# Optimization experiments

Hardware: AMD Instinct MI355X
Metric: run time of the kernel (lower is better)

Reference implementation:

```python
import jax, jax.numpy as jnp
import numpy as np

B, S, D = 4, 2048, 1024
E, H, TOPK = 8, 4096, 2


def setup_inputs() -> dict:
    key = jax.random.key(0)
    ks = jax.random.split(key, 6)
    scale_d = 1.0 / np.sqrt(D)
    scale_h = 1.0 / np.sqrt(H)
    return {
        "x": jax.random.normal(ks[0], (B, S, D), dtype=jnp.float32),
        "gate_w": jax.random.normal(ks[1], (D, E), dtype=jnp.float32) * scale_d,
        "w1": jax.random.normal(ks[2], (E, D, H), dtype=jnp.float32) * scale_d,
        "b1": jnp.zeros((E, H), dtype=jnp.float32),
        "w2": jax.random.normal(ks[3], (E, H, D), dtype=jnp.float32) * scale_h,
        "b2": jnp.zeros((E, D), dtype=jnp.float32),
    }


def reference(x, gate_w, w1, b1, w2, b2):
    # Gate: logits [B, S, E], top-k routing, softmax over the k selected logits
    gate_logits = jnp.einsum("bsd,de->bse", x, gate_w)
    topw, sel = jax.lax.top_k(gate_logits, TOPK)          # [B, S, K]
    topw = jax.nn.softmax(topw.astype(jnp.float32), axis=-1).astype(x.dtype)

    out = jnp.zeros_like(x)
    # Loop over the small, fixed expert set (structurally distinct params).
    for i in range(E):
        # combine weight for expert i per token (0 if not routed to i)
        coef = jnp.sum(jnp.where(sel == i, topw, jnp.zeros((), x.dtype)), axis=-1)  # [B, S]
        h = jax.nn.gelu(jnp.einsum("bsd,dh->bsh", x, w1[i]) + b1[i])
        y = jnp.einsum("bsh,hd->bsd", h, w2[i]) + b2[i]
        out = out + coef[..., None] * y
    return out
```

## Files before the change

kernel.cpp:

```cpp
#include <hip/hip_runtime.h>
#include <hip/hip_bf16.h>

#define T_TOKENS 8192
#define D_DIM 1024
#define H_DIM 4096
#define E_NUM 8
#define CAP 8192
#define CNT_PAD 16

#define TPB_G 32
#define GATE_BLKS (T_TOKENS / TPB_G)
#define TRW1_BLKS ((D_DIM / 64) * (H_DIM / 64) * E_NUM)
#define TRW2_BLKS ((H_DIM / 64) * (D_DIM / 64) * E_NUM)

typedef short bf16x8 __attribute__((ext_vector_type(8)));
typedef float f32x4 __attribute__((ext_vector_type(4)));
typedef unsigned short u16x8 __attribute__((ext_vector_type(8)));

__device__ inline unsigned short f2bf(float f) {
    __hip_bfloat16 h = __float2bfloat16(f);
    return *reinterpret_cast<unsigned short*>(&h);
}

__device__ inline float gelu_sig(float v) {
    float x = v * (1.5957691216057308f + 0.07135481627f * v * v);
    return v * __builtin_amdgcn_rcpf(1.0f + __expf(-x));
}

__device__ inline void gld_lds16(const unsigned short* g, unsigned short* lds) {
    __builtin_amdgcn_global_load_lds(
        (const __attribute__((address_space(1))) void*)g,
        (__attribute__((address_space(3))) void*)lds, 16, 0, 0);
}

#define WAITV0 do { asm volatile("s_waitcnt vmcnt(0)" ::: "memory"); \
                    __builtin_amdgcn_sched_barrier(0); } while (0)
#define SBAR   do { __builtin_amdgcn_sched_barrier(0); \
                    __builtin_amdgcn_s_barrier(); \
                    __builtin_amdgcn_sched_barrier(0); } while (0)

#define XCD_ITEMS(T)                                                          \
    int xcd = blockIdx.x & 7;                                                 \
    int lb  = blockIdx.x >> 3;                                                \
    int nbx = gridDim.x >> 3;                                                 \
    int q_ = (T) >> 3, r_ = (T) & 7;                                          \
    int base_ = (xcd < r_) ? xcd * (q_ + 1) : r_ * (q_ + 1) + (xcd - r_) * q_;\
    int cntx_ = (xcd < r_) ? q_ + 1 : q_;

__device__ inline void trw_body(const float* __restrict__ w,
                                unsigned short* __restrict__ wt,
                                int K, int N, int bb,
                                unsigned short (*tb)[72]) {
    int nk = K / 64, nn = N / 64;
    int e = bb / (nk * nn);
    int rem = bb - e * (nk * nn);
    int k0 = (rem % nk) * 64;
    int n0 = (rem / nk) * 64;
    const float* we = w + (size_t)e * K * N + (size_t)k0 * N + n0;
    unsigned short* wte = wt + (size_t)e * K * N + (size_t)n0 * K + k0;
    int tid = threadIdx.x;

    int kg = tid >> 4;
    int nq = (tid & 15) * 4;
    float4 r0 = *(const float4*)(we + (size_t)(kg * 4 + 0) * N + nq);
    float4 r1 = *(const float4*)(we + (size_t)(kg * 4 + 1) * N + nq);
    float4 r2 = *(const float4*)(we + (size_t)(kg * 4 + 2) * N + nq);
    float4 r3 = *(const float4*)(we + (size_t)(kg * 4 + 3) * N + nq);
    ushort4 u;
    u.x = f2bf(r0.x); u.y = f2bf(r1.x); u.z = f2bf(r2.x); u.w = f2bf(r3.x);
    *(ushort4*)&tb[nq + 0][kg * 4] = u;
    u.x = f2bf(r0.y); u.y = f2bf(r1.y); u.z = f2bf(r2.y); u.w = f2bf(r3.y);
    *(ushort4*)&tb[nq + 1][kg * 4] = u;
    u.x = f2bf(r0.z); u.y = f2bf(r1.z); u.z = f2bf(r2.z); u.w = f2bf(r3.z);
    *(ushort4*)&tb[nq + 2][kg * 4] = u;
    u.x = f2bf(r0.w); u.y = f2bf(r1.w); u.z = f2bf(r2.w); u.w = f2bf(r3.w);
    *(ushort4*)&tb[nq + 3][kg * 4] = u;

    __syncthreads();

#pragma unroll
    for (int p = 0; p < 2; ++p) {
        int n = p * 32 + (tid >> 3);
        int kc = (tid & 7) * 8;
        u16x8 v = *(const u16x8*)&tb[n][kc];
        *(u16x8*)(wte + (size_t)n * K + kc) = v;
    }
}

__global__ __launch_bounds__(256) void prep_kernel(const float* __restrict__ x,
                                                   const float* __restrict__ gw,
                                                   const float* __restrict__ w1,
                                                   const float* __restrict__ w2,
                                                   int* __restrict__ cnt,
                                                   int* __restrict__ tok,
                                                   float* __restrict__ cf,
                                                   unsigned short* __restrict__ xb,
                                                   unsigned short* __restrict__ w1t,
                                                   unsigned short* __restrict__ w2t) {
    __shared__ __align__(16) unsigned short tb[64][72];
    __shared__ int ls0[TPB_G], ls1[TPB_G];
    __shared__ float lp0[TPB_G], lp1[TPB_G];
    int b = blockIdx.x;
    if (b >= GATE_BLKS) {
        int bb = b - GATE_BLKS;
        if (bb < TRW1_BLKS) trw_body(w1, w1t, D_DIM, H_DIM, bb, tb);
        else                trw_body(w2, w2t, H_DIM, D_DIM, bb - TRW1_BLKS, tb);
        return;
    }
    int tid = threadIdx.x;
    int lane = tid & 63, wv = tid >> 6;
#pragma unroll
    for (int rep = 0; rep < TPB_G / 4; ++rep) {
        int ti = rep * 4 + wv;
        int t = b * TPB_G + ti;
        const float* xr = x + (size_t)t * D_DIM;
        unsigned short* xbr = xb + (size_t)t * D_DIM;
        double acc[E_NUM];
#pragma unroll
        for (int e = 0; e < E_NUM; ++e) acc[e] = 0.0;
#pragma unroll
        for (int it = 0; it < 4; ++it) {
            int d = it * 256 + lane * 4;
            float4 v = *(const float4*)(xr + d);
            ushort4 u;
            u.x = f2bf(v.x); u.y = f2bf(v.y); u.z = f2bf(v.z); u.w = f2bf(v.w);
            *(ushort4*)(xbr + d) = u;
            const float vv[4] = {v.x, v.y, v.z, v.w};
#pragma unroll
            for (int j = 0; j < 4; ++j) {
                const float* g = gw + (size_t)(d + j) * E_NUM;
#pragma unroll
                for (int e = 0; e < E_NUM; ++e) acc[e] += (double)vv[j] * (double)g[e];
            }
        }
#pragma unroll
        for (int e = 0; e < E_NUM; ++e) {
            double v = acc[e];
#pragma unroll
            for (int off = 32; off >= 1; off >>= 1) v += __shfl_xor(v, off);
            acc[e] = v;
        }
        if (lane == 0) {
            int s0 = 0;
#pragma unroll
            for (int e = 1; e < E_NUM; ++e) if (acc[e] > acc[s0]) s0 = e;
            int s1 = -1;
#pragma unroll
            for (int e = 0; e < E_NUM; ++e) if (e != s0 && (s1 < 0 || acc[e] > acc[s1])) s1 = e;
            float l0 = (float)acc[s0], l1 = (float)acc[s1];
            float p1 = __expf(l1 - l0);
            float inv = 1.0f / (1.0f + p1);
            ls0[ti] = s0; ls1[ti] = s1;
            lp0[ti] = inv; lp1[ti] = p1 * inv;
        }
    }
    __syncthreads();
    if (tid < E_NUM) {
        int e = tid, c = 0;
#pragma unroll
        for (int i = 0; i < TPB_G; ++i) c += (ls0[i] == e) + (ls1[i] == e);
        if (c > 0) {
            int q = atomicAdd(&cnt[e * CNT_PAD], c);
            for (int i = 0; i < TPB_G; ++i) {
                int t = b * TPB_G + i;
                if (ls0[i] == e) { tok[e * CAP + q] = t; cf[e * CAP + q] = lp0[i]; ++q; }
                if (ls1[i] == e) { tok[e * CAP + q] = t; cf[e * CAP + q] = lp1[i]; ++q; }
            }
        }
    }
}

__global__ __launch_bounds__(256, 2) void gemm1_fast(const unsigned short* __restrict__ xb,
                                                     const unsigned short* __restrict__ w1t,
                                                     const float* __restrict__ b1,
                                                     const int* __restrict__ cnt,
                                                     const int* __restrict__ tok,
                                                     unsigned short* __restrict__ Hbuf) {
    __shared__ __align__(16) unsigned short As0[128][64], As1[128][64];
    __shared__ __align__(16) unsigned short Bs0[128][64], Bs1[128][64];
    __shared__ int s_tok[128];

    int tid = threadIdx.x, lane = tid & 63, wv = tid >> 6;
    int wr = (wv >> 1) * 64, wc = (wv & 1) * 64;
    int lm = lane & 15, lk = lane >> 4;
    int srow = lane >> 3;
    int schunk = ((lane & 7) ^ srow) << 3;

    int ne_[E_NUM], offs_[E_NUM], pref[E_NUM + 1];
    pref[0] = 0;
    int off = 0;
#pragma unroll
    for (int e = 0; e < E_NUM; ++e) {
        ne_[e] = cnt[e * CNT_PAD];
        offs_[e] = off; off += ne_[e];
        pref[e + 1] = pref[e] + ((ne_[e] + 127) >> 7) * 32;
    }
    int T = pref[E_NUM];

    XCD_ITEMS(T)
    for (int ii = lb; ii < cntx_; ii += nbx) {
        int w = base_ + ii;
        int e = 0;
#pragma unroll
        for (int q = 0; q < E_NUM - 1; ++q) e += (w >= pref[q + 1]) ? 1 : 0;
        int local = w - pref[e];
        int bm0 = (local >> 5) * 128;
        int n0 = (local & 31) * 128;
        int ne = ne_[e];
        int offs = offs_[e];
        const unsigned short* w1e = w1t + (size_t)e * H_DIM * D_DIM;

        __syncthreads();
        if (tid < 128) s_tok[tid] = tok[e * CAP + min(bm0 + tid, ne - 1)];
        __syncthreads();

        const unsigned short* gA[4];
        const unsigned short* gB[4];
#pragma unroll
        for (int l = 0; l < 4; ++l) {
            gA[l] = xb + (size_t)s_tok[wv * 32 + l * 8 + srow] * D_DIM + schunk;
            gB[l] = w1e + (size_t)(n0 + wv * 32 + l * 8 + srow) * D_DIM + schunk;
        }
        float bias_v[4];
#pragma unroll
        for (int j = 0; j < 4; ++j) bias_v[j] = b1[(size_t)e * H_DIM + n0 + wc + j * 16 + lm];

        f32x4 acc[4][4];
#pragma unroll
        for (int i = 0; i < 4; ++i)
#pragma unroll
            for (int j = 0; j < 4; ++j) { f32x4 z = {0.f, 0.f, 0.f, 0.f}; acc[i][j] = z; }

        auto STAGE = [&](unsigned short (&A)[128][64], unsigned short (&B)[128][64], int kb) {
            int k0 = kb * 64;
#pragma unroll
            for (int l = 0; l < 4; ++l) gld_lds16(gA[l] + k0, &A[wv * 32 + l * 8][0]);
#pragma unroll
            for (int l = 0; l < 4; ++l) gld_lds16(gB[l] + k0, &B[wv * 32 + l * 8][0]);
        };
        auto COMPUTE = [&](unsigned short (&A)[128][64], unsigned short (&B)[128][64]) {
#pragma unroll
            for (int ks = 0; ks < 2; ++ks) {
                bf16x8 a[4], b[4];
                int c = (((ks * 4 + lk) ^ (lm & 7)) << 3);
#pragma unroll
                for (int f = 0; f < 4; ++f) a[f] = *(const bf16x8*)&A[wr + f * 16 + lm][c];
#pragma unroll
                for (int f = 0; f < 4; ++f) b[f] = *(const bf16x8*)&B[wc + f * 16 + lm][c];
                __builtin_amdgcn_s_setprio(1);
#pragma unroll
                for (int i = 0; i < 4; ++i)
#pragma unroll
                    for (int j = 0; j < 4; ++j)
                        acc[i][j] = __builtin_amdgcn_mfma_f32_16x16x32_bf16(a[i], b[j], acc[i][j], 0, 0, 0);
                __builtin_amdgcn_s_setprio(0);
            }
        };

        const int NT = D_DIM / 64;
        STAGE(As0, Bs0, 0);
        WAITV0; SBAR;
        for (int t = 0; t < NT; t += 2) {
            if (t + 1 < NT) STAGE(As1, Bs1, t + 1);
            COMPUTE(As0, Bs0);
            WAITV0; SBAR;
            if (t + 2 < NT) STAGE(As0, Bs0, t + 2);
            COMPUTE(As1, Bs1);
            WAITV0; SBAR;
        }

#pragma unroll
        for (int i = 0; i < 4; ++i) {
#pragma unroll
            for (int r = 0; r < 4; ++r) {
                int row = wr + i * 16 + lk * 4 + r;
                int gr = bm0 + row;
                if (gr >= ne) continue;
                size_t rb = (size_t)(offs + gr) * H_DIM;
#pragma unroll
                for (int j = 0; j < 4; ++j) {
                    int gn = n0 + wc + j * 16 + lm;
                    float v = acc[i][j][r] + bias_v[j];
                    Hbuf[rb + gn] = f2bf(gelu_sig(v));
                }
            }
        }
    }
}

__global__ __launch_bounds__(256, 2) void gemm2_fast(const unsigned short* __restrict__ Hbuf,
                                                     const unsigned short* __restrict__ w2t,
                                                     const float* __restrict__ b2,
                                                     const int* __restrict__ cnt,
                                                     const int* __restrict__ tok,
                                                     const float* __restrict__ cf,
                                                     float* __restrict__ out) {
    __shared__ __align__(16) unsigned short As0[128][64], As1[128][64];
    __shared__ __align__(16) unsigned short Bs0[128][64], Bs1[128][64];
    __shared__ int s_tok[128];
    __shared__ float s_cf[128];

    int tid = threadIdx.x, lane = tid & 63, wv = tid >> 6;
    int wr = (wv >> 1) * 64, wc = (wv & 1) * 64;
    int lm = lane & 15, lk = lane >> 4;
    int srow = lane >> 3;
    int schunk = ((lane & 7) ^ srow) << 3;

    int ne_[E_NUM], offs_[E_NUM], pref[E_NUM + 1];
    pref[0] = 0;
    int off = 0;
#pragma unroll
    for (int e = 0; e < E_NUM; ++e) {
        ne_[e] = cnt[e * CNT_PAD];
        offs_[e] = off; off += ne_[e];
        pref[e + 1] = pref[e] + ((ne_[e] + 127) >> 7) * 8;
    }
    int T = pref[E_NUM];

    XCD_ITEMS(T)
    for (int ii = lb; ii < cntx_; ii += nbx) {
        int w = base_ + ii;
        int e = 0;
#pragma unroll
        for (int q = 0; q < E_NUM - 1; ++q) e += (w >= pref[q + 1]) ? 1 : 0;
        int local = w - pref[e];
        int bm0 = (local >> 3) * 128;
        int n0 = (local & 7) * 128;
        int ne = ne_[e];
        int offs = offs_[e];
        const unsigned short* w2e = w2t + (size_t)e * H_DIM * D_DIM;

        __syncthreads();
        if (tid < 128) {
            int gi = min(bm0 + tid, ne - 1);
            s_tok[tid] = tok[e * CAP + gi];
            s_cf[tid] = cf[e * CAP + gi];
        }
        __syncthreads();

        const unsigned short* gA[4];
        const unsigned short* gB[4];
#pragma unroll
        for (int l = 0; l < 4; ++l) {
            gA[l] = Hbuf + (size_t)(offs + min(bm0 + wv * 32 + l * 8 + srow, ne - 1)) * H_DIM + schunk;
            gB[l] = w2e + (size_t)(n0 + wv * 32 + l * 8 + srow) * H_DIM + schunk;
        }
        float bias_v[4];
#pragma unroll
        for (int j = 0; j < 4; ++j) bias_v[j] = b2[(size_t)e * D_DIM + n0 + wc + j * 16 + lm];

        f32x4 acc[4][4];
#pragma unroll
        for (int i = 0; i < 4; ++i)
#pragma unroll
            for (int j = 0; j < 4; ++j) { f32x4 z = {0.f, 0.f, 0.f, 0.f}; acc[i][j] = z; }

        auto STAGE = [&](unsigned short (&A)[128][64], unsigned short (&B)[128][64], int kb) {
            int k0 = kb * 64;
#pragma unroll
            for (int l = 0; l < 4; ++l) gld_lds16(gA[l] + k0, &A[wv * 32 + l * 8][0]);
#pragma unroll
            for (int l = 0; l < 4; ++l) gld_lds16(gB[l] + k0, &B[wv * 32 + l * 8][0]);
        };
        auto COMPUTE = [&](unsigned short (&A)[128][64], unsigned short (&B)[128][64]) {
#pragma unroll
            for (int ks = 0; ks < 2; ++ks) {
                bf16x8 a[4], b[4];
                int c = (((ks * 4 + lk) ^ (lm & 7)) << 3);
#pragma unroll
                for (int f = 0; f < 4; ++f) a[f] = *(const bf16x8*)&A[wr + f * 16 + lm][c];
#pragma unroll
                for (int f = 0; f < 4; ++f) b[f] = *(const bf16x8*)&B[wc + f * 16 + lm][c];
                __builtin_amdgcn_s_setprio(1);
#pragma unroll
                for (int i = 0; i < 4; ++i)
#pragma unroll
                    for (int j = 0; j < 4; ++j)
                        acc[i][j] = __builtin_amdgcn_mfma_f32_16x16x32_bf16(a[i], b[j], acc[i][j], 0, 0, 0);
                __builtin_amdgcn_s_setprio(0);
            }
        };

        const int NT = H_DIM / 64;
        STAGE(As0, Bs0, 0);
        WAITV0; SBAR;
        for (int t = 0; t < NT; t += 2) {
            if (t + 1 < NT) STAGE(As1, Bs1, t + 1);
            COMPUTE(As0, Bs0);
            WAITV0; SBAR;
            if (t + 2 < NT) STAGE(As0, Bs0, t + 2);
            COMPUTE(As1, Bs1);
            WAITV0; SBAR;
        }

#pragma unroll
        for (int i = 0; i < 4; ++i) {
#pragma unroll
            for (int r = 0; r < 4; ++r) {
                int row = wr + i * 16 + lk * 4 + r;
                int gr = bm0 + row;
                if (gr >= ne) continue;
                int tk = s_tok[row];
                float cw = s_cf[row];
#pragma unroll
                for (int j = 0; j < 4; ++j) {
                    int gn = n0 + wc + j * 16 + lm;
                    float y = acc[i][j][r] + bias_v[j];
                    atomicAdd(&out[(size_t)tk * D_DIM + gn], cw * y);
                }
            }
        }
    }
}

extern "C" void kernel_launch(void* const* d_in, const int* in_sizes, int n_in,
                              void* d_out, int out_size, void* d_ws, size_t ws_size,
                              hipStream_t stream) {
    const float* x  = (const float*)d_in[0];
    const float* gw = (const float*)d_in[1];
    const float* w1 = (const float*)d_in[2];
    const float* b1 = (const float*)d_in[3];
    const float* w2 = (const float*)d_in[4];
    const float* b2 = (const float*)d_in[5];
    float* out = (float*)d_out;

    char* ws = (char*)d_ws;
    const size_t SZ_CNT   = E_NUM * CNT_PAD * 4;
    const size_t SZ_ROUTE = SZ_CNT + (size_t)2 * E_NUM * CAP * 4;
    const size_t SZ_XB    = (size_t)T_TOKENS * D_DIM * 2;
    const size_t SZ_W     = (size_t)E_NUM * D_DIM * H_DIM * 2;
    const size_t SZ_H     = (size_t)2 * T_TOKENS * H_DIM * 2;

    int*   cnt = (int*)ws;
    int*   tok = (int*)(ws + SZ_CNT);
    float* cff = (float*)(ws + SZ_CNT + E_NUM * CAP * 4);

    size_t need_fast = SZ_ROUTE + SZ_XB + 2 * SZ_W + SZ_H;
    if (ws_size < need_fast) return;

    unsigned short* xb   = (unsigned short*)(ws + SZ_ROUTE);
    unsigned short* w1t  = (unsigned short*)(ws + SZ_ROUTE + SZ_XB);
    unsigned short* w2t  = (unsigned short*)(ws + SZ_ROUTE + SZ_XB + SZ_W);
    unsigned short* Hbuf = (unsigned short*)(ws + SZ_ROUTE + SZ_XB + 2 * SZ_W);

    hipMemsetAsync(cnt, 0, SZ_CNT, stream);
    hipMemsetAsync(out, 0, (size_t)out_size * sizeof(float), stream);

    prep_kernel<<<GATE_BLKS + TRW1_BLKS + TRW2_BLKS, 256, 0, stream>>>(
        x, gw, w1, w2, cnt, tok, cff, xb, w1t, w2t);

    gemm1_fast<<<512, 256, 0, stream>>>(xb, w1t, b1, cnt, tok, Hbuf);
    gemm2_fast<<<512, 256, 0, stream>>>(Hbuf, w2t, b2, cnt, tok, cff, out);
}
```

Baseline: 580.6 us.

## Use 256x256 tiles with 8 waves and triple-buffered K=32 LDS pipeline

```diff
diff --git a/kernel.cpp b/kernel.cpp
--- a/kernel.cpp
+++ b/kernel.cpp
@@ -33,11 +33,13 @@
         (__attribute__((address_space(3))) void*)lds, 16, 0, 0);
 }
 
-#define WAITV0 do { asm volatile("s_waitcnt vmcnt(0)" ::: "memory"); \
-                    __builtin_amdgcn_sched_barrier(0); } while (0)
-#define SBAR   do { __builtin_amdgcn_sched_barrier(0); \
-                    __builtin_amdgcn_s_barrier(); \
-                    __builtin_amdgcn_sched_barrier(0); } while (0)
+#define WAITV(N) do { asm volatile("s_waitcnt vmcnt(" #N ")" ::: "memory"); \
+                      __builtin_amdgcn_sched_barrier(0); } while (0)
+#define LGKM0    do { asm volatile("s_waitcnt lgkmcnt(0)" ::: "memory"); \
+                      __builtin_amdgcn_sched_barrier(0); } while (0)
+#define SBAR     do { __builtin_amdgcn_sched_barrier(0); \
+                      __builtin_amdgcn_s_barrier(); \
+                      __builtin_amdgcn_sched_barrier(0); } while (0)
 
 #define XCD_ITEMS(T)                                                          \
     int xcd = blockIdx.x & 7;                                                 \
@@ -170,21 +172,23 @@
     }
 }
 
-__global__ __launch_bounds__(256, 2) void gemm1_fast(const unsigned short* __restrict__ xb,
+
+__global__ __launch_bounds__(512, 2) void gemm1_fast(const unsigned short* __restrict__ xb,
                                                      const unsigned short* __restrict__ w1t,
                                                      const float* __restrict__ b1,
                                                      const int* __restrict__ cnt,
                                                      const int* __restrict__ tok,
                                                      unsigned short* __restrict__ Hbuf) {
-    __shared__ __align__(16) unsigned short As0[128][64], As1[128][64];
-    __shared__ __align__(16) unsigned short Bs0[128][64], Bs1[128][64];
-    __shared__ int s_tok[128];
+    __shared__ __align__(16) unsigned short As[3][256][32];
+    __shared__ __align__(16) unsigned short Bs[3][256][32];
+    __shared__ int s_tok[256];
 
     int tid = threadIdx.x, lane = tid & 63, wv = tid >> 6;
-    int wr = (wv >> 1) * 64, wc = (wv & 1) * 64;
-    int lm = lane & 15, lk = lane >> 4;
-    int srow = lane >> 3;
-    int schunk = ((lane & 7) ^ srow) << 3;
+    int wm = wv >> 2, wn = wv & 3;
+    int lm = lane & 15, lkq = lane >> 4;
+    int srow = tid >> 2;
+    int schunk = (((tid & 3) ^ (srow & 3)) << 3);
+    int rdc = ((lkq ^ (lm & 3)) << 3);
 
     int ne_[E_NUM], offs_[E_NUM], pref[E_NUM + 1];
     pref[0] = 0;
@@ -193,7 +197,7 @@
     for (int e = 0; e < E_NUM; ++e) {
         ne_[e] = cnt[e * CNT_PAD];
         offs_[e] = off; off += ne_[e];
-        pref[e + 1] = pref[e] + ((ne_[e] + 127) >> 7) * 32;
+        pref[e + 1] = pref[e] + ((ne_[e] + 255) >> 8) * 16;
     }
     int T = pref[E_NUM];
 
@@ -204,82 +208,93 @@
 #pragma unroll
         for (int q = 0; q < E_NUM - 1; ++q) e += (w >= pref[q + 1]) ? 1 : 0;
         int local = w - pref[e];
-        int bm0 = (local >> 5) * 128;
-        int n0 = (local & 31) * 128;
+        int bm0 = (local >> 4) * 256;
+        int n0 = (local & 15) * 256;
         int ne = ne_[e];
         int offs = offs_[e];
         const unsigned short* w1e = w1t + (size_t)e * H_DIM * D_DIM;
 
         __syncthreads();
-        if (tid < 128) s_tok[tid] = tok[e * CAP + min(bm0 + tid, ne - 1)];
+        if (tid < 256) s_tok[tid] = tok[e * CAP + min(bm0 + tid, ne - 1)];
         __syncthreads();
 
-        const unsigned short* gA[4];
-        const unsigned short* gB[4];
-#pragma unroll
-        for (int l = 0; l < 4; ++l) {
-            gA[l] = xb + (size_t)s_tok[wv * 32 + l * 8 + srow] * D_DIM + schunk;
-            gB[l] = w1e + (size_t)(n0 + wv * 32 + l * 8 + srow) * D_DIM + schunk;
+        const unsigned short* gA[2];
+        const unsigned short* gB[2];
+#pragma unroll
+        for (int u = 0; u < 2; ++u) {
+            gA[u] = xb + (size_t)s_tok[u * 128 + srow] * D_DIM + schunk;
+            gB[u] = w1e + (size_t)(n0 + u * 128 + srow) * D_DIM + schunk;
         }
         float bias_v[4];
 #pragma unroll
-        for (int j = 0; j < 4; ++j) bias_v[j] = b1[(size_t)e * H_DIM + n0 + wc + j * 16 + lm];
-
-        f32x4 acc[4][4];
-#pragma unroll
-        for (int i = 0; i < 4; ++i)
+        for (int j = 0; j < 4; ++j)
+            bias_v[j] = b1[(size_t)e * H_DIM + n0 + wn * 64 + j * 16 + lm];
+
+        f32x4 acc[8][4];
+#pragma unroll
+        for (int i = 0; i < 8; ++i)
 #pragma unroll
             for (int j = 0; j < 4; ++j) { f32x4 z = {0.f, 0.f, 0.f, 0.f}; acc[i][j] = z; }
 
-        auto STAGE = [&](unsigned short (&A)[128][64], unsigned short (&B)[128][64], int kb) {
-            int k0 = kb * 64;
-#pragma unroll
-            for (int l = 0; l < 4; ++l) gld_lds16(gA[l] + k0, &A[wv * 32 + l * 8][0]);
-#pragma unroll
-            for (int l = 0; l < 4; ++l) gld_lds16(gB[l] + k0, &B[wv * 32 + l * 8][0]);
+        auto STAGE_A = [&](int sl, int kb, int u) {
+            gld_lds16(gA[u] + kb * 32, &As[sl][u * 128 + wv * 16][0]);
         };
-        auto COMPUTE = [&](unsigned short (&A)[128][64], unsigned short (&B)[128][64]) {
-#pragma unroll
-            for (int ks = 0; ks < 2; ++ks) {
-                bf16x8 a[4], b[4];
-                int c = (((ks * 4 + lk) ^ (lm & 7)) << 3);
-#pragma unroll
-                for (int f = 0; f < 4; ++f) a[f] = *(const bf16x8*)&A[wr + f * 16 + lm][c];
-#pragma unroll
-                for (int f = 0; f < 4; ++f) b[f] = *(const bf16x8*)&B[wc + f * 16 + lm][c];
-                __builtin_amdgcn_s_setprio(1);
-#pragma unroll
-                for (int i = 0; i < 4; ++i)
-#pragma unroll
-                    for (int j = 0; j < 4; ++j)
-                        acc[i][j] = __builtin_amdgcn_mfma_f32_16x16x32_bf16(a[i], b[j], acc[i][j], 0, 0, 0);
-                __builtin_amdgcn_s_setprio(0);
-            }
+        auto STAGE_B = [&](int sl, int kb, int u) {
+            gld_lds16(gB[u] + kb * 32, &Bs[sl][u * 128 + wv * 16][0]);
         };
 
-        const int NT = D_DIM / 64;
-        STAGE(As0, Bs0, 0);
-        WAITV0; SBAR;
-        for (int t = 0; t < NT; t += 2) {
-            if (t + 1 < NT) STAGE(As1, Bs1, t + 1);
-            COMPUTE(As0, Bs0);
-            WAITV0; SBAR;
-            if (t + 2 < NT) STAGE(As0, Bs0, t + 2);
-            COMPUTE(As1, Bs1);
-            WAITV0; SBAR;
-        }
-
-#pragma unroll
-        for (int i = 0; i < 4; ++i) {
+        const int NT = D_DIM / 32;
+        STAGE_A(0, 0, 0); STAGE_A(0, 0, 1); STAGE_B(0, 0, 0); STAGE_B(0, 0, 1);
+        STAGE_A(1, 1, 0); STAGE_A(1, 1, 1); STAGE_B(1, 1, 0); STAGE_B(1, 1, 1);
+
+        int s = 0, s2 = 2;
+        for (int t = 0; t < NT; ++t) {
+            if (t + 1 < NT) { WAITV(4); } else { WAITV(0); }
+            SBAR;
+            bf16x8 bfr[4], afr[4];
+#pragma unroll
+            for (int f = 0; f < 4; ++f)
+                bfr[f] = *(const bf16x8*)&Bs[s][wn * 64 + f * 16 + lm][rdc];
+#pragma unroll
+            for (int f = 0; f < 4; ++f)
+                afr[f] = *(const bf16x8*)&As[s][wm * 128 + f * 16 + lm][rdc];
+            if (t + 2 < NT) { STAGE_A(s2, t + 2, 0); STAGE_A(s2, t + 2, 1); }
+            LGKM0;
+            __builtin_amdgcn_s_setprio(1);
+#pragma unroll
+            for (int i = 0; i < 4; ++i)
+#pragma unroll
+                for (int j = 0; j < 4; ++j)
+                    acc[i][j] = __builtin_amdgcn_mfma_f32_16x16x32_bf16(afr[i], bfr[j], acc[i][j], 0, 0, 0);
+            __builtin_amdgcn_s_setprio(0);
+#pragma unroll
+            for (int f = 0; f < 4; ++f)
+                afr[f] = *(const bf16x8*)&As[s][wm * 128 + 64 + f * 16 + lm][rdc];
+            if (t + 2 < NT) { STAGE_B(s2, t + 2, 0); STAGE_B(s2, t + 2, 1); }
+            LGKM0;
+            __builtin_amdgcn_s_setprio(1);
+#pragma unroll
+            for (int i = 0; i < 4; ++i)
+#pragma unroll
+                for (int j = 0; j < 4; ++j)
+                    acc[4 + i][j] = __builtin_amdgcn_mfma_f32_16x16x32_bf16(afr[i], bfr[j], acc[4 + i][j], 0, 0, 0);
+            __builtin_amdgcn_s_setprio(0);
+            s = (s == 2) ? 0 : s + 1;
+            s2 = (s2 == 2) ? 0 : s2 + 1;
+        }
+
+#pragma unroll
+        for (int i = 0; i < 8; ++i) {
+            int frow = wm * 128 + ((i < 4) ? i * 16 : 64 + (i - 4) * 16);
 #pragma unroll
             for (int r = 0; r < 4; ++r) {
-                int row = wr + i * 16 + lk * 4 + r;
+                int row = frow + lkq * 4 + r;
                 int gr = bm0 + row;
                 if (gr >= ne) continue;
                 size_t rb = (size_t)(offs + gr) * H_DIM;
 #pragma unroll
                 for (int j = 0; j < 4; ++j) {
-                    int gn = n0 + wc + j * 16 + lm;
+                    int gn = n0 + wn * 64 + j * 16 + lm;
                     float v = acc[i][j][r] + bias_v[j];
                     Hbuf[rb + gn] = f2bf(gelu_sig(v));
                 }
@@ -288,23 +303,24 @@
     }
 }
 
-__global__ __launch_bounds__(256, 2) void gemm2_fast(const unsigned short* __restrict__ Hbuf,
+__global__ __launch_bounds__(512, 2) void gemm2_fast(const unsigned short* __restrict__ Hbuf,
                                                      const unsigned short* __restrict__ w2t,
                                                      const float* __restrict__ b2,
                                                      const int* __restrict__ cnt,
                                                      const int* __restrict__ tok,
                                                      const float* __restrict__ cf,
                                                      float* __restrict__ out) {
-    __shared__ __align__(16) unsigned short As0[128][64], As1[128][64];
-    __shared__ __align__(16) unsigned short Bs0[128][64], Bs1[128][64];
-    __shared__ int s_tok[128];
-    __shared__ float s_cf[128];
+    __shared__ __align__(16) unsigned short As[3][256][32];
+    __shared__ __align__(16) unsigned short Bs[3][256][32];
+    __shared__ int s_tok[256];
+    __shared__ float s_cf[256];
 
     int tid = threadIdx.x, lane = tid & 63, wv = tid >> 6;
-    int wr = (wv >> 1) * 64, wc = (wv & 1) * 64;
-    int lm = lane & 15, lk = lane >> 4;
-    int srow = lane >> 3;
-    int schunk = ((lane & 7) ^ srow) << 3;
+    int wm = wv >> 2, wn = wv & 3;
+    int lm = lane & 15, lkq = lane >> 4;
+    int srow = tid >> 2;
+    int schunk = (((tid & 3) ^ (srow & 3)) << 3);
+    int rdc = ((lkq ^ (lm & 3)) << 3);
 
     int ne_[E_NUM], offs_[E_NUM], pref[E_NUM + 1];
     pref[0] = 0;
@@ -313,7 +329,7 @@
     for (int e = 0; e < E_NUM; ++e) {
         ne_[e] = cnt[e * CNT_PAD];
         offs_[e] = off; off += ne_[e];
-        pref[e + 1] = pref[e] + ((ne_[e] + 127) >> 7) * 8;
+        pref[e + 1] = pref[e] + ((ne_[e] + 255) >> 8) * 4;
     }
     int T = pref[E_NUM];
 
@@ -324,87 +340,98 @@
 #pragma unroll
         for (int q = 0; q < E_NUM - 1; ++q) e += (w >= pref[q + 1]) ? 1 : 0;
         int local = w - pref[e];
-        int bm0 = (local >> 3) * 128;
-        int n0 = (local & 7) * 128;
+        int bm0 = (local >> 2) * 256;
+        int n0 = (local & 3) * 256;
         int ne = ne_[e];
         int offs = offs_[e];
         const unsigned short* w2e = w2t + (size_t)e * H_DIM * D_DIM;
 
         __syncthreads();
-        if (tid < 128) {
+        if (tid < 256) {
             int gi = min(bm0 + tid, ne - 1);
             s_tok[tid] = tok[e * CAP + gi];
             s_cf[tid] = cf[e * CAP + gi];
         }
         __syncthreads();
 
-        const unsigned short* gA[4];
-        const unsigned short* gB[4];
-#pragma unroll
-        for (int l = 0; l < 4; ++l) {
-            gA[l] = Hbuf + (size_t)(offs + min(bm0 + wv * 32 + l * 8 + srow, ne - 1)) * H_DIM + schunk;
-            gB[l] = w2e + (size_t)(n0 + wv * 32 + l * 8 + srow) * H_DIM + schunk;
+        const unsigned short* gA[2];
+        const unsigned short* gB[2];
+#pragma unroll
+        for (int u = 0; u < 2; ++u) {
+            gA[u] = Hbuf + (size_t)(offs + min(bm0 + u * 128 + srow, ne - 1)) * H_DIM + schunk;
+            gB[u] = w2e + (size_t)(n0 + u * 128 + srow) * H_DIM + schunk;
         }
         float bias_v[4];
 #pragma unroll
-        for (int j = 0; j < 4; ++j) bias_v[j] = b2[(size_t)e * D_DIM + n0 + wc + j * 16 + lm];
-
-        f32x4 acc[4][4];
-#pragma unroll
-        for (int i = 0; i < 4; ++i)
+        for (int j = 0; j < 4; ++j)
+            bias_v[j] = b2[(size_t)e * D_DIM + n0 + wn * 64 + j * 16 + lm];
+
+        f32x4 acc[8][4];
+#pragma unroll
+        for (int i = 0; i < 8; ++i)
 #pragma unroll
             for (int j = 0; j < 4; ++j) { f32x4 z = {0.f, 0.f, 0.f, 0.f}; acc[i][j] = z; }
 
-        auto STAGE = [&](unsigned short (&A)[128][64], unsigned short (&B)[128][64], int kb) {
-            int k0 = kb * 64;
-#pragma unroll
-            for (int l = 0; l < 4; ++l) gld_lds16(gA[l] + k0, &A[wv * 32 + l * 8][0]);
-#pragma unroll
-            for (int l = 0; l < 4; ++l) gld_lds16(gB[l] + k0, &B[wv * 32 + l * 8][0]);
+        auto STAGE_A = [&](int sl, int kb, int u) {
+            gld_lds16(gA[u] + kb * 32, &As[sl][u * 128 + wv * 16][0]);
         };
-        auto COMPUTE = [&](unsigned short (&A)[128][64], unsigned short (&B)[128][64]) {
-#pragma unroll
-            for (int ks = 0; ks < 2; ++ks) {
-                bf16x8 a[4], b[4];
-                int c = (((ks * 4 + lk) ^ (lm & 7)) << 3);
-#pragma unroll
-                for (int f = 0; f < 4; ++f) a[f] = *(const bf16x8*)&A[wr + f * 16 + lm][c];
-#pragma unroll
-                for (int f = 0; f < 4; ++f) b[f] = *(const bf16x8*)&B[wc + f * 16 + lm][c];
-                __builtin_amdgcn_s_setprio(1);
-#pragma unroll
-                for (int i = 0; i < 4; ++i)
-#pragma unroll
-                    for (int j = 0; j < 4; ++j)
-                        acc[i][j] = __builtin_amdgcn_mfma_f32_16x16x32_bf16(a[i], b[j], acc[i][j], 0, 0, 0);
-                __builtin_amdgcn_s_setprio(0);
-            }
+        auto STAGE_B = [&](int sl, int kb, int u) {
+            gld_lds16(gB[u] + kb * 32, &Bs[sl][u * 128 + wv * 16][0]);
         };
 
-        const int NT = H_DIM / 64;
-        STAGE(As0, Bs0, 0);
-        WAITV0; SBAR;
-        for (int t = 0; t < NT; t += 2) {
-            if (t + 1 < NT) STAGE(As1, Bs1, t + 1);
-            COMPUTE(As0, Bs0);
-            WAITV0; SBAR;
-            if (t + 2 < NT) STAGE(As0, Bs0, t + 2);
-            COMPUTE(As1, Bs1);
-            WAITV0; SBAR;
-        }
-
-#pragma unroll
-        for (int i = 0; i < 4; ++i) {
+        const int NT = H_DIM / 32;
+        STAGE_A(0, 0, 0); STAGE_A(0, 0, 1); STAGE_B(0, 0, 0); STAGE_B(0, 0, 1);
+        STAGE_A(1, 1, 0); STAGE_A(1, 1, 1); STAGE_B(1, 1, 0); STAGE_B(1, 1, 1);
+
+        int s = 0, s2 = 2;
+        for (int t = 0; t < NT; ++t) {
+            if (t + 1 < NT) { WAITV(4); } else { WAITV(0); }
+            SBAR;
+            bf16x8 bfr[4], afr[4];
+#pragma unroll
+            for (int f = 0; f < 4; ++f)
+                bfr[f] = *(const bf16x8*)&Bs[s][wn * 64 + f * 16 + lm][rdc];
+#pragma unroll
+            for (int f = 0; f < 4; ++f)
+                afr[f] = *(const bf16x8*)&As[s][wm * 128 + f * 16 + lm][rdc];
+            if (t + 2 < NT) { STAGE_A(s2, t + 2, 0); STAGE_A(s2, t + 2, 1); }
+            LGKM0;
+            __builtin_amdgcn_s_setprio(1);
+#pragma unroll
+            for (int i = 0; i < 4; ++i)
+#pragma unroll
+                for (int j = 0; j < 4; ++j)
+                    acc[i][j] = __builtin_amdgcn_mfma_f32_16x16x32_bf16(afr[i], bfr[j], acc[i][j], 0, 0, 0);
+            __builtin_amdgcn_s_setprio(0);
+#pragma unroll
+            for (int f = 0; f < 4; ++f)
+                afr[f] = *(const bf16x8*)&As[s][wm * 128 + 64 + f * 16 + lm][rdc];
+            if (t + 2 < NT) { STAGE_B(s2, t + 2, 0); STAGE_B(s2, t + 2, 1); }
+            LGKM0;
+            __builtin_amdgcn_s_setprio(1);
+#pragma unroll
+            for (int i = 0; i < 4; ++i)
+#pragma unroll
+                for (int j = 0; j < 4; ++j)
+                    acc[4 + i][j] = __builtin_amdgcn_mfma_f32_16x16x32_bf16(afr[i], bfr[j], acc[4 + i][j], 0, 0, 0);
+            __builtin_amdgcn_s_setprio(0);
+            s = (s == 2) ? 0 : s + 1;
+            s2 = (s2 == 2) ? 0 : s2 + 1;
+        }
+
+#pragma unroll
+        for (int i = 0; i < 8; ++i) {
+            int frow = wm * 128 + ((i < 4) ? i * 16 : 64 + (i - 4) * 16);
 #pragma unroll
             for (int r = 0; r < 4; ++r) {
-                int row = wr + i * 16 + lk * 4 + r;
+                int row = frow + lkq * 4 + r;
                 int gr = bm0 + row;
                 if (gr >= ne) continue;
                 int tk = s_tok[row];
                 float cw = s_cf[row];
 #pragma unroll
                 for (int j = 0; j < 4; ++j) {
-                    int gn = n0 + wc + j * 16 + lm;
+                    int gn = n0 + wn * 64 + j * 16 + lm;
                     float y = acc[i][j][r] + bias_v[j];
                     atomicAdd(&out[(size_t)tk * D_DIM + gn], cw * y);
                 }
@@ -449,6 +476,6 @@
     prep_kernel<<<GATE_BLKS + TRW1_BLKS + TRW2_BLKS, 256, 0, stream>>>(
         x, gw, w1, w2, cnt, tok, cff, xb, w1t, w2t);
 
-    gemm1_fast<<<512, 256, 0, stream>>>(xb, w1t, b1, cnt, tok, Hbuf);
-    gemm2_fast<<<512, 256, 0, stream>>>(Hbuf, w2t, b2, cnt, tok, cff, out);
-}
+    gemm1_fast<<<256, 512, 0, stream>>>(xb, w1t, b1, cnt, tok, Hbuf);
+    gemm2_fast<<<256, 512, 0, stream>>>(Hbuf, w2t, b2, cnt, tok, cff, out);
+}
```

Measured after the change: 614.1 us. 1.06x slower.
